# Performance work log

Hardware: AMD Instinct MI355X
Metric: run time of the kernel (lower is better)

Reference implementation:

```python
import jax, jax.numpy as jnp
import numpy as np

OMEGA = 32  # recall threshold from init_kwargs


def setup_inputs() -> dict:
    key = jax.random.key(0)
    B, T, F, H = 32, 1024, 256, 256
    stdv = 1.0 / np.sqrt(H).astype(np.float32)
    ks = jax.random.split(key, 10)
    u = lambda k, shape: jax.random.uniform(k, shape, jnp.float32, -stdv, stdv)
    return {
        "x": jax.random.normal(ks[0], (B, T, F), jnp.float32),
        "W": u(ks[1], (F, 4 * H)),
        "U": u(ks[2], (H, 4 * H)),
        "P": u(ks[3], (B, 2 * B)),
        "B_bias": u(ks[4], (4 * H,)),
        "W_r": u(ks[5], (F, 1)),
        "P_r": u(ks[6], (1, B)),
        "U_r": u(ks[7], (H, 1)),
        "W_out": u(ks[8], (H, 1)),
        "b_out": u(ks[9], (1,)),
    }


def reference(x, W, U, P, B_bias, W_r, P_r, U_r, W_out, b_out):
    Bsz, T, F = x.shape
    H = U.shape[0]
    xs = jnp.swapaxes(x, 0, 1)  # [T, B, F]
    h0 = jnp.zeros((Bsz, H), x.dtype)
    c0 = jnp.zeros((Bsz, H), x.dtype)
    Xm0 = jnp.zeros((T, Bsz, F), x.dtype)  # states_array: stored x_t per step
    Hm0 = jnp.zeros((T, Bsz, H), x.dtype)  # states_array: stored h_t per step

    def step(carry, inp):
        h, c, Xm, Hm = carry
        x_t, t = inp  # x_t: [B, F], t: scalar int (== len(states_array) before append)
        # recall gate: sigmoid(P_r @ (x_t @ W_r + h @ U_r)) -> [1,1]
        gate = jax.nn.sigmoid(P_r @ (x_t @ W_r + h @ U_r))[0, 0]
        # best index = round(t * gate); clip to valid range (source would IndexError at t)
        idx = jnp.clip(jnp.round(t.astype(x.dtype) * gate).astype(jnp.int32), 0, jnp.maximum(t - 1, 0))
        use_self = t < OMEGA
        x_rec = jnp.where(use_self, x_t, Xm[idx])
        h_rec = jnp.where(use_self, h, Hm[idx])
        # append current (x_t, h_t) to the memory bank
        Xm = Xm.at[t].set(x_t)
        Hm = Hm.at[t].set(h)
        # x_t_prime = [x_t; x_rec] (2B rows); fold the vstack into a concat of the two affine maps
        a_cur = x_t @ W + h @ U      # [B, 4H]
        a_rec = x_rec @ W + h_rec @ U  # [B, 4H]
        gates = P @ jnp.concatenate([a_cur, a_rec], axis=0) + B_bias  # [B, 4H]
        i_t, f_t, g_t, _o_raw = jnp.split(gates, 4, axis=1)
        i_t = jax.nn.sigmoid(i_t)
        f_t = jax.nn.sigmoid(f_t)
        g_t = jnp.tanh(g_t)
        o_t = i_t  # faithful to source: o_t = sigmoid(i chunk), not the o chunk
        c = f_t * c + i_t * g_t
        h = o_t * jnp.tanh(c)
        return (h, c, Xm, Hm), None

    (h, c, _, _), _ = jax.lax.scan(step, (h0, c0, Xm0, Hm0), (xs, jnp.arange(T)))
    return h @ W_out + b_out  # [B, 1]
```

## Files before the change

kernel.cpp:

```cpp
#include <hip/hip_runtime.h>
#include <cstdint>
#include <cstddef>


#define T_STEPS 1024
#define BSZ 32
#define FDIM 256
#define HDIM 256
#define G3W 384
#define KWG 64
#define HS 4
#define JC 12
#define HPAD 260
#define OMEGA 32
#define HSLICE 8192

static const size_t AXC_BYTES = (size_t)KWG * T_STEPS * G3W * sizeof(float);
static const size_t HB_BYTES  = (size_t)(T_STEPS + 1) * HSLICE * sizeof(float);
static const size_t GX_BYTES  = (size_t)T_STEPS * sizeof(double);
static const size_t GP_BYTES  = (size_t)(T_STEPS + 1) * 128 * sizeof(double);

__device__ __forceinline__ uint32_t uminv(uint32_t a, uint32_t b) {
  return a < b ? a : b;
}

__global__ __launch_bounds__(256) void phaseA(const float* __restrict__ x,
                                              const float* __restrict__ W,
                                              const float* __restrict__ W_r,
                                              const float* __restrict__ P_r,
                                              float* __restrict__ AXc,
                                              double* __restrict__ gx) {
  const int t = blockIdx.x;
  const int tid = threadIdx.x;
  __shared__ __align__(16) float xs[BSZ][HPAD];
  __shared__ double sred[BSZ];

  for (int i = tid; i < BSZ * FDIM / 4; i += 256) {
    const int b = (i * 4) >> 8;
    const int k = (i * 4) & 255;
    *(float4*)&xs[b][k] = *(const float4*)&x[((size_t)b * T_STEPS + t) * FDIM + k];
  }
  __syncthreads();

  for (int pass = 0; pass < 3; ++pass) {
    const int j = pass * 256 + tid;
    float acc[BSZ];
#pragma unroll
    for (int b = 0; b < BSZ; ++b) acc[b] = 0.f;
    for (int k0 = 0; k0 < FDIM; k0 += 4) {
      const float w0 = W[(size_t)(k0 + 0) * 1024 + j];
      const float w1 = W[(size_t)(k0 + 1) * 1024 + j];
      const float w2 = W[(size_t)(k0 + 2) * 1024 + j];
      const float w3 = W[(size_t)(k0 + 3) * 1024 + j];
#pragma unroll
      for (int b = 0; b < BSZ; ++b) {
        const float4 xv = *(const float4*)&xs[b][k0];
        acc[b] = fmaf(xv.x, w0, acc[b]);
        acc[b] = fmaf(xv.y, w1, acc[b]);
        acc[b] = fmaf(xv.z, w2, acc[b]);
        acc[b] = fmaf(xv.w, w3, acc[b]);
      }
    }
    const int wgj = (j >> 2) & 63;
    const int slot = ((j >> 8) << 2) | (j & 3);
    float* dst = AXc + ((size_t)wgj * T_STEPS + t) * G3W + slot;
    for (int b = 0; b < BSZ; ++b) dst[b * 12] = acc[b];
  }

  if (tid < BSZ) {
    double s = 0.0;
    for (int k = 0; k < FDIM; k += 4) {
      const float4 xv = *(const float4*)&xs[tid][k];
      const float4 wv = *(const float4*)&W_r[k];
      s = fma((double)xv.x, (double)wv.x, s);
      s = fma((double)xv.y, (double)wv.y, s);
      s = fma((double)xv.z, (double)wv.z, s);
      s = fma((double)xv.w, (double)wv.w, s);
    }
    sred[tid] = s;
  }
  __syncthreads();
  if (tid == 0) {
    double g = 0.0;
    for (int b = 0; b < BSZ; ++b) g = fma((double)P_r[b], sred[b], g);
    gx[t] = g;
  }
}

__global__ __launch_bounds__(256) void phaseB(const float* __restrict__ U,
                                              const float* __restrict__ P,
                                              const float* __restrict__ B_bias,
                                              const float* __restrict__ P_r,
                                              const float* __restrict__ U_r,
                                              float* __restrict__ AXc,
                                              float* __restrict__ hbank,
                                              const double* __restrict__ gx,
                                              double* __restrict__ gp) {
  const int wg = blockIdx.x;
  const int tid = threadIdx.x;
  const int lane = tid & 63;

  __shared__ __align__(16) float ULt[JC][HPAD];
  __shared__ __align__(16) float hL[BSZ][HPAD];
  __shared__ __align__(16) float PL[BSZ][64];
  __shared__ __align__(16) float acs[JC][36];
  __shared__ __align__(16) float ars[JC][36];
  __shared__ __align__(16) float red1[BSZ][JC];
  __shared__ float biasL[JC];

  for (int i = tid; i < JC * HDIM; i += 256) {
    const int jc = i >> 8, k = i & 255;
    const int col = (jc >> 2) * HDIM + wg * HS + (jc & 3);
    ULt[jc][k] = U[(size_t)k * 1024 + col];
  }
  for (int i = tid; i < BSZ * 64; i += 256) PL[i >> 6][i & 63] = P[i];
  if (tid < JC) biasL[tid] = B_bias[(tid >> 2) * HDIM + wg * HS + (tid & 3)];

  double wgt = 0.0;
  if (tid < 128) {
    wgt = (double)P_r[tid >> 2] * (double)U_r[wg * HS + (tid & 3)];
  }

  const int u = (tid >= 64) ? (tid - 64) : 0;
  const int khalf = u / 96;
  const int rmap = u % 96;
  const int jcp = rmap % 6, bA = rmap / 6;
  const int jc0 = 2 * jcp, jc1 = jc0 + 1;
  const int bB = bA + 16;
  const int kb = khalf * 128;

  const int ob = tid >> 2, ohc = tid & 3;
  const int grow = tid & 31;
  const int gc0 = (tid >> 5) * 4;

  float* __restrict__ AXwg = AXc + (size_t)wg * T_STEPS * G3W;

  float creg = 0.f;
  __syncthreads();

  for (int t = 0; t < T_STEPS; ++t) {
    float2 xwA = {0.f, 0.f}, xwB = {0.f, 0.f};
    size_t aA = 0, aB = 0;
    if (tid >= 64 && tid < 160) {
      aA = (size_t)t * G3W + bA * JC + jc0;
      aB = (size_t)t * G3W + bB * JC + jc0;
      xwA = *(const float2*)&AXwg[aA];
      xwB = *(const float2*)&AXwg[aB];
    }
    double gxt = 0.0;
    if (tid == 0) gxt = gx[t];

    {
      const uint64_t base =
          (uint64_t)(hbank + (size_t)t * HSLICE) + (uint64_t)tid * 16u;
      const uint64_t a0 = base;
      const uint64_t a1 = base + 4096u;
      const uint64_t a2 = base + 8192u;
      const uint64_t a3 = base + 12288u;
      const uint64_t a4 = base + 16384u;
      const uint64_t a5 = base + 20480u;
      const uint64_t a6 = base + 24576u;
      const uint64_t a7 = base + 28672u;
      float4 r0, r1, r2, r3, r4, r5, r6, r7;
      int guard = 0;
      for (;;) {
        asm volatile(
            "global_load_dwordx4 %0, %8, off sc0 sc1\n\t"
            "global_load_dwordx4 %1, %9, off sc0 sc1\n\t"
            "global_load_dwordx4 %2, %10, off sc0 sc1\n\t"
            "global_load_dwordx4 %3, %11, off sc0 sc1\n\t"
            "global_load_dwordx4 %4, %12, off sc0 sc1\n\t"
            "global_load_dwordx4 %5, %13, off sc0 sc1\n\t"
            "global_load_dwordx4 %6, %14, off sc0 sc1\n\t"
            "global_load_dwordx4 %7, %15, off sc0 sc1\n\t"
            "s_waitcnt vmcnt(0)"
            : "=&v"(r0), "=&v"(r1), "=&v"(r2), "=&v"(r3),
              "=&v"(r4), "=&v"(r5), "=&v"(r6), "=&v"(r7)
            : "v"(a0), "v"(a1), "v"(a2), "v"(a3),
              "v"(a4), "v"(a5), "v"(a6), "v"(a7)
            : "memory");
        uint32_t m = 0xFFFFFFFFu;
#define CHK(f) m = uminv(m, ~__float_as_uint(f))
        CHK(r0.x); CHK(r0.y); CHK(r0.z); CHK(r0.w);
        CHK(r1.x); CHK(r1.y); CHK(r1.z); CHK(r1.w);
        CHK(r2.x); CHK(r2.y); CHK(r2.z); CHK(r2.w);
        CHK(r3.x); CHK(r3.y); CHK(r3.z); CHK(r3.w);
        CHK(r4.x); CHK(r4.y); CHK(r4.z); CHK(r4.w);
        CHK(r5.x); CHK(r5.y); CHK(r5.z); CHK(r5.w);
        CHK(r6.x); CHK(r6.y); CHK(r6.z); CHK(r6.w);
        CHK(r7.x); CHK(r7.y); CHK(r7.z); CHK(r7.w);
#undef CHK
        if (m != 0u) break;
        if (++guard > (1 << 16)) break;
        __builtin_amdgcn_s_sleep(1);
      }
      *(float4*)&hL[grow][gc0 + 0]   = r0;
      *(float4*)&hL[grow][gc0 + 32]  = r1;
      *(float4*)&hL[grow][gc0 + 64]  = r2;
      *(float4*)&hL[grow][gc0 + 96]  = r3;
      *(float4*)&hL[grow][gc0 + 128] = r4;
      *(float4*)&hL[grow][gc0 + 160] = r5;
      *(float4*)&hL[grow][gc0 + 192] = r6;
      *(float4*)&hL[grow][gc0 + 224] = r7;
    }
    __syncthreads();

    float s00 = 0.f, s01 = 0.f, s10 = 0.f, s11 = 0.f;
    if (tid < 64) {
      if (t >= OMEGA) {
        const uint64_t ga0 = (uint64_t)(gp + (size_t)t * 128 + lane);
        const uint64_t ga1 = ga0 + 512u;
        double d0, d1;
        int guard = 0;
        for (;;) {
          asm volatile(
              "global_load_dwordx2 %0, %2, off sc0 sc1\n\t"
              "global_load_dwordx2 %1, %3, off sc0 sc1\n\t"
              "s_waitcnt vmcnt(0)"
              : "=&v"(d0), "=&v"(d1)
              : "v"(ga0), "v"(ga1)
              : "memory");
          const int ok = (__double_as_longlong(d0) != -1ll) &&
                         (__double_as_longlong(d1) != -1ll);
          if (__all(ok)) break;
          if (++guard > (1 << 16)) break;
          __builtin_amdgcn_s_sleep(1);
        }
        double v = d0 + d1;
        v += __shfl_xor(v, 32, 64);
        v += __shfl_xor(v, 16, 64);
        v += __shfl_xor(v, 8, 64);
        v += __shfl_xor(v, 4, 64);
        v += __shfl_xor(v, 2, 64);
        v += __shfl_xor(v, 1, 64);
        int idx = 0;
        if (tid == 0) {
          const double g = gxt + v;
          const double gate = 1.0 / (1.0 + exp(-g));
          idx = (int)rint((double)t * gate);
          if (idx > t - 1) idx = t - 1;
          if (idx < 0) idx = 0;
        }
        idx = __shfl(idx, 0, 64);
        const float* __restrict__ src = AXwg + (size_t)idx * G3W;
        float av[6];
#pragma unroll
        for (int j = 0; j < 6; ++j) av[j] = src[lane + j * 64];
#pragma unroll
        for (int j = 0; j < 6; ++j) {
          const int f = lane + j * 64;
          ars[f % JC][f / JC] = av[j];
        }
      }
    } else {
      for (int k = kb; k < kb + 128; k += 4) {
        const float4 u0 = *(const float4*)&ULt[jc0][k];
        const float4 u1 = *(const float4*)&ULt[jc1][k];
        const float4 h0 = *(const float4*)&hL[bA][k];
        const float4 h1 = *(const float4*)&hL[bB][k];
        s00 = fmaf(h0.x, u0.x, s00); s00 = fmaf(h0.y, u0.y, s00);
        s00 = fmaf(h0.z, u0.z, s00); s00 = fmaf(h0.w, u0.w, s00);
        s01 = fmaf(h0.x, u1.x, s01); s01 = fmaf(h0.y, u1.y, s01);
        s01 = fmaf(h0.z, u1.z, s01); s01 = fmaf(h0.w, u1.w, s01);
        s10 = fmaf(h1.x, u0.x, s10); s10 = fmaf(h1.y, u0.y, s10);
        s10 = fmaf(h1.z, u0.z, s10); s10 = fmaf(h1.w, u0.w, s10);
        s11 = fmaf(h1.x, u1.x, s11); s11 = fmaf(h1.y, u1.y, s11);
        s11 = fmaf(h1.z, u1.z, s11); s11 = fmaf(h1.w, u1.w, s11);
      }
      if (khalf == 1) {
        *(float2*)&red1[bA][jc0] = make_float2(s00, s01);
        *(float2*)&red1[bB][jc0] = make_float2(s10, s11);
      }
    }
    __syncthreads();

    if (tid >= 64 && tid < 160) {
      const float2 rA = *(const float2*)&red1[bA][jc0];
      const float2 rB = *(const float2*)&red1[bB][jc0];
      const float v00 = s00 + rA.x + xwA.x;
      const float v01 = s01 + rA.y + xwA.y;
      const float v10 = s10 + rB.x + xwB.x;
      const float v11 = s11 + rB.y + xwB.y;
      *(float2*)&AXwg[aA] = make_float2(v00, v01);
      *(float2*)&AXwg[aB] = make_float2(v10, v11);
      acs[jc0][bA] = v00;  acs[jc1][bA] = v01;
      acs[jc0][bB] = v10;  acs[jc1][bB] = v11;
      if (t < OMEGA) {
        ars[jc0][bA] = v00;  ars[jc1][bA] = v01;
        ars[jc0][bB] = v10;  ars[jc1][bB] = v11;
      }
    }
    __syncthreads();

    if (tid < BSZ * HS) {
      float gi = biasL[ohc];
      float gf = biasL[4 + ohc];
      float gg = biasL[8 + ohc];
#pragma unroll
      for (int b4 = 0; b4 < BSZ; b4 += 4) {
        const float4 pv = *(const float4*)&PL[ob][b4];
        const float4 ai = *(const float4*)&acs[ohc][b4];
        const float4 af = *(const float4*)&acs[4 + ohc][b4];
        const float4 ag = *(const float4*)&acs[8 + ohc][b4];
        gi = fmaf(pv.x, ai.x, gi); gi = fmaf(pv.y, ai.y, gi);
        gi = fmaf(pv.z, ai.z, gi); gi = fmaf(pv.w, ai.w, gi);
        gf = fmaf(pv.x, af.x, gf); gf = fmaf(pv.y, af.y, gf);
        gf = fmaf(pv.z, af.z, gf); gf = fmaf(pv.w, af.w, gf);
        gg = fmaf(pv.x, ag.x, gg); gg = fmaf(pv.y, ag.y, gg);
        gg = fmaf(pv.z, ag.z, gg); gg = fmaf(pv.w, ag.w, gg);
      }
#pragma unroll
      for (int b4 = 0; b4 < BSZ; b4 += 4) {
        const float4 pv = *(const float4*)&PL[ob][BSZ + b4];
        const float4 ai = *(const float4*)&ars[ohc][b4];
        const float4 af = *(const float4*)&ars[4 + ohc][b4];
        const float4 ag = *(const float4*)&ars[8 + ohc][b4];
        gi = fmaf(pv.x, ai.x, gi); gi = fmaf(pv.y, ai.y, gi);
        gi = fmaf(pv.z, ai.z, gi); gi = fmaf(pv.w, ai.w, gi);
        gf = fmaf(pv.x, af.x, gf); gf = fmaf(pv.y, af.y, gf);
        gf = fmaf(pv.z, af.z, gf); gf = fmaf(pv.w, af.w, gf);
        gg = fmaf(pv.x, ag.x, gg); gg = fmaf(pv.y, ag.y, gg);
        gg = fmaf(pv.z, ag.z, gg); gg = fmaf(pv.w, ag.w, gg);
      }
      const float iv = 1.f / (1.f + expf(-gi));
      const float fv = 1.f / (1.f + expf(-gf));
      const float gv = tanhf(gg);
      creg = fmaf(fv, creg, iv * gv);
      const float hv = iv * tanhf(creg);
      const uint64_t daddr =
          (uint64_t)(hbank + (size_t)(t + 1) * HSLICE + (size_t)wg * (BSZ * HS)) +
          (uint64_t)tid * 4u;
      asm volatile("global_store_dword %0, %1, off sc0 sc1"
                   :: "v"(daddr), "v"(hv)
                   : "memory");
      double p = wgt * (double)hv;
      p += __shfl_xor(p, 32, 64);
      p += __shfl_xor(p, 16, 64);
      p += __shfl_xor(p, 8, 64);
      p += __shfl_xor(p, 4, 64);
      p += __shfl_xor(p, 2, 64);
      p += __shfl_xor(p, 1, 64);
      if (lane == 0) {
        const uint64_t pa =
            (uint64_t)(gp + (size_t)(t + 1) * 128 + (size_t)((tid >> 6) * 64 + wg));
        asm volatile("global_store_dwordx2 %0, %1, off sc0 sc1"
                     :: "v"(pa), "v"(p)
                     : "memory");
      }
    }
  }
}

__global__ void outK(const float* __restrict__ hbank, const float* __restrict__ W_out,
                     const float* __restrict__ b_out, float* __restrict__ out) {
  const int b = threadIdx.x;
  if (b < BSZ) {
    const float* h = hbank + (size_t)T_STEPS * HSLICE;
    float s = 0.f;
    for (int wg = 0; wg < KWG; ++wg) {
      const float4 hv = *(const float4*)&h[wg * (BSZ * HS) + b * HS];
      const float4 wv = *(const float4*)&W_out[wg * HS];
      s = fmaf(hv.x, wv.x, s); s = fmaf(hv.y, wv.y, s);
      s = fmaf(hv.z, wv.z, s); s = fmaf(hv.w, wv.w, s);
    }
    out[b] = s + b_out[0];
  }
}

extern "C" void kernel_launch(void* const* d_in, const int* in_sizes, int n_in,
                              void* d_out, int out_size, void* d_ws, size_t ws_size,
                              hipStream_t stream) {
  const float* x      = (const float*)d_in[0];
  const float* W      = (const float*)d_in[1];
  const float* U      = (const float*)d_in[2];
  const float* P      = (const float*)d_in[3];
  const float* B_bias = (const float*)d_in[4];
  const float* W_r    = (const float*)d_in[5];
  const float* P_r    = (const float*)d_in[6];
  const float* U_r    = (const float*)d_in[7];
  const float* W_out  = (const float*)d_in[8];
  const float* b_out  = (const float*)d_in[9];

  char* ws = (char*)d_ws;
  float*    AXc   = (float*)ws;
  float*    hbank = (float*)(ws + AXC_BYTES);
  double*   gx    = (double*)(ws + AXC_BYTES + HB_BYTES);
  double*   gp    = (double*)(ws + AXC_BYTES + HB_BYTES + GX_BYTES);

  hipMemsetAsync(hbank, 0xFF, HB_BYTES, stream);
  hipMemsetAsync(gp, 0xFF, GP_BYTES, stream);
  hipMemsetAsync(hbank, 0, (size_t)HSLICE * sizeof(float), stream);

  phaseA<<<T_STEPS, 256, 0, stream>>>(x, W, W_r, P_r, AXc, gx);
  phaseB<<<KWG, 256, 0, stream>>>(U, P, B_bias, P_r, U_r, AXc, hbank, gx, gp);
  outK<<<1, 64, 0, stream>>>(hbank, W_out, b_out, (float*)d_out);
}
```

Before: 5.008 ms.

## Split recurrent step across 128 workgroups with two hidden columns each

Doubles the number of persistent workgroups in the recurrent phase from 64 to 128, halving each workgroup's slice of hidden units (and gate columns) per step. The hidden-state bank is also reorganized to a natural [batch][hidden] layout so each workgroup writes strided single columns and readers load contiguous rows. This aims to cut per-step compute latency on the serial critical path by spreading work across more CUs. The cost is more cross-workgroup polling traffic and synchronization participants, plus many idle threads within each workgroup.

```diff
diff --git a/kernel.cpp b/kernel.cpp
--- a/kernel.cpp
+++ b/kernel.cpp
@@ -7,10 +7,10 @@
 #define BSZ 32
 #define FDIM 256
 #define HDIM 256
-#define G3W 384
-#define KWG 64
-#define HS 4
-#define JC 12
+#define KWG 128
+#define HS 2
+#define JC 6
+#define G3W 192
 #define HPAD 260
 #define OMEGA 32
 #define HSLICE 8192
@@ -18,7 +18,7 @@
 static const size_t AXC_BYTES = (size_t)KWG * T_STEPS * G3W * sizeof(float);
 static const size_t HB_BYTES  = (size_t)(T_STEPS + 1) * HSLICE * sizeof(float);
 static const size_t GX_BYTES  = (size_t)T_STEPS * sizeof(double);
-static const size_t GP_BYTES  = (size_t)(T_STEPS + 1) * 128 * sizeof(double);
+static const size_t GP_BYTES  = (size_t)(T_STEPS + 1) * KWG * sizeof(double);
 
 __device__ __forceinline__ uint32_t uminv(uint32_t a, uint32_t b) {
   return a < b ? a : b;
@@ -61,10 +61,10 @@
         acc[b] = fmaf(xv.w, w3, acc[b]);
       }
     }
-    const int wgj = (j >> 2) & 63;
-    const int slot = ((j >> 8) << 2) | (j & 3);
+    const int wgj = (j >> 1) & 127;
+    const int slot = ((j >> 8) << 1) | (j & 1);
     float* dst = AXc + ((size_t)wgj * T_STEPS + t) * G3W + slot;
-    for (int b = 0; b < BSZ; ++b) dst[b * 12] = acc[b];
+    for (int b = 0; b < BSZ; ++b) dst[b * JC] = acc[b];
   }
 
   if (tid < BSZ) {
@@ -102,36 +102,38 @@
 
   __shared__ __align__(16) float ULt[JC][HPAD];
   __shared__ __align__(16) float hL[BSZ][HPAD];
-  __shared__ __align__(16) float PL[BSZ][64];
+  __shared__ __align__(16) float PL[BSZ][68];
   __shared__ __align__(16) float acs[JC][36];
   __shared__ __align__(16) float ars[JC][36];
-  __shared__ __align__(16) float red1[BSZ][JC];
+  __shared__ __align__(16) float red1[BSZ][8];
   __shared__ float biasL[JC];
 
   for (int i = tid; i < JC * HDIM; i += 256) {
     const int jc = i >> 8, k = i & 255;
-    const int col = (jc >> 2) * HDIM + wg * HS + (jc & 3);
+    const int col = (jc >> 1) * HDIM + wg * HS + (jc & 1);
     ULt[jc][k] = U[(size_t)k * 1024 + col];
   }
   for (int i = tid; i < BSZ * 64; i += 256) PL[i >> 6][i & 63] = P[i];
-  if (tid < JC) biasL[tid] = B_bias[(tid >> 2) * HDIM + wg * HS + (tid & 3)];
-
-  double wgt = 0.0;
-  if (tid < 128) {
-    wgt = (double)P_r[tid >> 2] * (double)U_r[wg * HS + (tid & 3)];
-  }
-
-  const int u = (tid >= 64) ? (tid - 64) : 0;
-  const int khalf = u / 96;
-  const int rmap = u % 96;
-  const int jcp = rmap % 6, bA = rmap / 6;
+  if (tid < JC) biasL[tid] = B_bias[(tid >> 1) * HDIM + wg * HS + (tid & 1)];
+
+  const bool hu_act = (tid >= 64 && tid < 160);
+  const int u = hu_act ? (tid - 64) : 0;
+  const int khalf = u / 48;
+  const int rmap = u % 48;
+  const int jcp = rmap % 3, bA = rmap / 3;
   const int jc0 = 2 * jcp, jc1 = jc0 + 1;
   const int bB = bA + 16;
   const int kb = khalf * 128;
 
-  const int ob = tid >> 2, ohc = tid & 3;
-  const int grow = tid & 31;
-  const int gc0 = (tid >> 5) * 4;
+  const int o = (tid >= 192) ? (tid - 192) : 0;
+  const int ob = o >> 1, ohc = o & 1;
+  double wgt = 0.0;
+  if (tid >= 192) {
+    wgt = (double)P_r[ob] * (double)U_r[wg * HS + ohc];
+  }
+
+  const int gw4 = tid >> 6;
+  const int gcol = (tid & 63) * 4;
 
   float* __restrict__ AXwg = AXc + (size_t)wg * T_STEPS * G3W;
 
@@ -141,7 +143,7 @@
   for (int t = 0; t < T_STEPS; ++t) {
     float2 xwA = {0.f, 0.f}, xwB = {0.f, 0.f};
     size_t aA = 0, aB = 0;
-    if (tid >= 64 && tid < 160) {
+    if (tid >= 64 && tid < 112) {
       aA = (size_t)t * G3W + bA * JC + jc0;
       aB = (size_t)t * G3W + bB * JC + jc0;
       xwA = *(const float2*)&AXwg[aA];
@@ -194,21 +196,21 @@
         if (++guard > (1 << 16)) break;
         __builtin_amdgcn_s_sleep(1);
       }
-      *(float4*)&hL[grow][gc0 + 0]   = r0;
-      *(float4*)&hL[grow][gc0 + 32]  = r1;
-      *(float4*)&hL[grow][gc0 + 64]  = r2;
-      *(float4*)&hL[grow][gc0 + 96]  = r3;
-      *(float4*)&hL[grow][gc0 + 128] = r4;
-      *(float4*)&hL[grow][gc0 + 160] = r5;
-      *(float4*)&hL[grow][gc0 + 192] = r6;
-      *(float4*)&hL[grow][gc0 + 224] = r7;
+      *(float4*)&hL[0 * 4 + gw4][gcol] = r0;
+      *(float4*)&hL[1 * 4 + gw4][gcol] = r1;
+      *(float4*)&hL[2 * 4 + gw4][gcol] = r2;
+      *(float4*)&hL[3 * 4 + gw4][gcol] = r3;
+      *(float4*)&hL[4 * 4 + gw4][gcol] = r4;
+      *(float4*)&hL[5 * 4 + gw4][gcol] = r5;
+      *(float4*)&hL[6 * 4 + gw4][gcol] = r6;
+      *(float4*)&hL[7 * 4 + gw4][gcol] = r7;
     }
     __syncthreads();
 
     float s00 = 0.f, s01 = 0.f, s10 = 0.f, s11 = 0.f;
     if (tid < 64) {
       if (t >= OMEGA) {
-        const uint64_t ga0 = (uint64_t)(gp + (size_t)t * 128 + lane);
+        const uint64_t ga0 = (uint64_t)(gp + (size_t)t * KWG + lane);
         const uint64_t ga1 = ga0 + 512u;
         double d0, d1;
         int guard = 0;
@@ -243,16 +245,16 @@
         }
         idx = __shfl(idx, 0, 64);
         const float* __restrict__ src = AXwg + (size_t)idx * G3W;
-        float av[6];
-#pragma unroll
-        for (int j = 0; j < 6; ++j) av[j] = src[lane + j * 64];
-#pragma unroll
-        for (int j = 0; j < 6; ++j) {
+        float av[3];
+#pragma unroll
+        for (int j = 0; j < 3; ++j) av[j] = src[lane + j * 64];
+#pragma unroll
+        for (int j = 0; j < 3; ++j) {
           const int f = lane + j * 64;
           ars[f % JC][f / JC] = av[j];
         }
       }
-    } else {
+    } else if (hu_act) {
       for (int k = kb; k < kb + 128; k += 4) {
         const float4 u0 = *(const float4*)&ULt[jc0][k];
         const float4 u1 = *(const float4*)&ULt[jc1][k];
@@ -274,7 +276,7 @@
     }
     __syncthreads();
 
-    if (tid >= 64 && tid < 160) {
+    if (tid >= 64 && tid < 112) {
       const float2 rA = *(const float2*)&red1[bA][jc0];
       const float2 rB = *(const float2*)&red1[bB][jc0];
       const float v00 = s00 + rA.x + xwA.x;
@@ -292,16 +294,16 @@
     }
     __syncthreads();
 
-    if (tid < BSZ * HS) {
+    if (tid >= 192) {
       float gi = biasL[ohc];
-      float gf = biasL[4 + ohc];
-      float gg = biasL[8 + ohc];
+      float gf = biasL[2 + ohc];
+      float gg = biasL[4 + ohc];
 #pragma unroll
       for (int b4 = 0; b4 < BSZ; b4 += 4) {
         const float4 pv = *(const float4*)&PL[ob][b4];
         const float4 ai = *(const float4*)&acs[ohc][b4];
-        const float4 af = *(const float4*)&acs[4 + ohc][b4];
-        const float4 ag = *(const float4*)&acs[8 + ohc][b4];
+        const float4 af = *(const float4*)&acs[2 + ohc][b4];
+        const float4 ag = *(const float4*)&acs[4 + ohc][b4];
         gi = fmaf(pv.x, ai.x, gi); gi = fmaf(pv.y, ai.y, gi);
         gi = fmaf(pv.z, ai.z, gi); gi = fmaf(pv.w, ai.w, gi);
         gf = fmaf(pv.x, af.x, gf); gf = fmaf(pv.y, af.y, gf);
@@ -313,8 +315,8 @@
       for (int b4 = 0; b4 < BSZ; b4 += 4) {
         const float4 pv = *(const float4*)&PL[ob][BSZ + b4];
         const float4 ai = *(const float4*)&ars[ohc][b4];
-        const float4 af = *(const float4*)&ars[4 + ohc][b4];
-        const float4 ag = *(const float4*)&ars[8 + ohc][b4];
+        const float4 af = *(const float4*)&ars[2 + ohc][b4];
+        const float4 ag = *(const float4*)&ars[4 + ohc][b4];
         gi = fmaf(pv.x, ai.x, gi); gi = fmaf(pv.y, ai.y, gi);
         gi = fmaf(pv.z, ai.z, gi); gi = fmaf(pv.w, ai.w, gi);
         gf = fmaf(pv.x, af.x, gf); gf = fmaf(pv.y, af.y, gf);
@@ -328,8 +330,8 @@
       creg = fmaf(fv, creg, iv * gv);
       const float hv = iv * tanhf(creg);
       const uint64_t daddr =
-          (uint64_t)(hbank + (size_t)(t + 1) * HSLICE + (size_t)wg * (BSZ * HS)) +
-          (uint64_t)tid * 4u;
+          (uint64_t)(hbank + (size_t)(t + 1) * HSLICE +
+                     (size_t)ob * HDIM + (size_t)wg * HS + ohc) ;
       asm volatile("global_store_dword %0, %1, off sc0 sc1"
                    :: "v"(daddr), "v"(hv)
                    : "memory");
@@ -341,8 +343,7 @@
       p += __shfl_xor(p, 2, 64);
       p += __shfl_xor(p, 1, 64);
       if (lane == 0) {
-        const uint64_t pa =
-            (uint64_t)(gp + (size_t)(t + 1) * 128 + (size_t)((tid >> 6) * 64 + wg));
+        const uint64_t pa = (uint64_t)(gp + (size_t)(t + 1) * KWG + wg);
         asm volatile("global_store_dwordx2 %0, %1, off sc0 sc1"
                      :: "v"(pa), "v"(p)
                      : "memory");
@@ -355,11 +356,11 @@
                      const float* __restrict__ b_out, float* __restrict__ out) {
   const int b = threadIdx.x;
   if (b < BSZ) {
-    const float* h = hbank + (size_t)T_STEPS * HSLICE;
+    const float* h = hbank + (size_t)T_STEPS * HSLICE + (size_t)b * HDIM;
     float s = 0.f;
-    for (int wg = 0; wg < KWG; ++wg) {
-      const float4 hv = *(const float4*)&h[wg * (BSZ * HS) + b * HS];
-      const float4 wv = *(const float4*)&W_out[wg * HS];
+    for (int c = 0; c < HDIM; c += 4) {
+      const float4 hv = *(const float4*)&h[c];
+      const float4 wv = *(const float4*)&W_out[c];
       s = fmaf(hv.x, wv.x, s); s = fmaf(hv.y, wv.y, s);
       s = fmaf(hv.z, wv.z, s); s = fmaf(hv.w, wv.w, s);
     }
```

After: 8.445 ms. +68.6%, slower.

## Prefetch next step's hidden-state slice on idle threads and pad LDS rows

Applied to the files above, without the earlier changes.

The spin-wait gather of the full h slice from the global bank moves off the start of every step. Threads 128-255, which take no part in publishing h, now run it at the end of the previous step. Each of these threads issues twice as many 16-byte acquire loads, covering the work the full block did before. The shared arrays hL and PL get wider row padding, presumably to cut LDS bank conflicts. This aims to shorten the serial critical path of each recurrent step, but it depends on hL no longer being read by other threads when the early gather overwrites it.

```diff
diff --git a/kernel.cpp b/kernel.cpp
--- a/kernel.cpp
+++ b/kernel.cpp
@@ -12,6 +12,7 @@
 #define HS 4
 #define JC 12
 #define HPAD 260
+#define HPADH 276
 #define OMEGA 32
 #define HSLICE 8192
 
@@ -101,8 +102,8 @@
   const int lane = tid & 63;
 
   __shared__ __align__(16) float ULt[JC][HPAD];
-  __shared__ __align__(16) float hL[BSZ][HPAD];
-  __shared__ __align__(16) float PL[BSZ][64];
+  __shared__ __align__(16) float hL[BSZ][HPADH];
+  __shared__ __align__(16) float PL[BSZ][68];
   __shared__ __align__(16) float acs[JC][36];
   __shared__ __align__(16) float ars[JC][36];
   __shared__ __align__(16) float red1[BSZ][JC];
@@ -130,13 +131,89 @@
   const int kb = khalf * 128;
 
   const int ob = tid >> 2, ohc = tid & 3;
-  const int grow = tid & 31;
-  const int gc0 = (tid >> 5) * 4;
+  const int tp = (tid >= 128) ? (tid - 128) : 0;
+  const int grow = tp & 31;
+  const int gc0 = (tp >> 5) * 4;
 
   float* __restrict__ AXwg = AXc + (size_t)wg * T_STEPS * G3W;
 
   float creg = 0.f;
   __syncthreads();
+
+#define GATHER_SLICE(TS)                                                       \
+  {                                                                            \
+    const uint64_t base =                                                      \
+        (uint64_t)(hbank + (size_t)(TS)*HSLICE) + (uint64_t)tp * 16u;          \
+    const uint64_t a0 = base;                                                  \
+    const uint64_t a1 = base + 4096u;                                          \
+    const uint64_t a2 = base + 8192u;                                          \
+    const uint64_t a3 = base + 12288u;                                         \
+    const uint64_t a4 = base + 16384u;                                         \
+    const uint64_t a5 = base + 20480u;                                         \
+    const uint64_t a6 = base + 24576u;                                         \
+    const uint64_t a7 = base + 28672u;                                         \
+    float4 r0, r1, r2, r3, r4, r5, r6, r7;                                     \
+    float4 s0, s1, s2, s3, s4, s5, s6, s7;                                     \
+    int guard = 0;                                                             \
+    for (;;) {                                                                 \
+      asm volatile(                                                            \
+          "global_load_dwordx4 %0, %16, off sc0 sc1\n\t"                       \
+          "global_load_dwordx4 %1, %16, off offset:2048 sc0 sc1\n\t"           \
+          "global_load_dwordx4 %2, %17, off sc0 sc1\n\t"                       \
+          "global_load_dwordx4 %3, %17, off offset:2048 sc0 sc1\n\t"           \
+          "global_load_dwordx4 %4, %18, off sc0 sc1\n\t"                       \
+          "global_load_dwordx4 %5, %18, off offset:2048 sc0 sc1\n\t"           \
+          "global_load_dwordx4 %6, %19, off sc0 sc1\n\t"                       \
+          "global_load_dwordx4 %7, %19, off offset:2048 sc0 sc1\n\t"           \
+          "global_load_dwordx4 %8, %20, off sc0 sc1\n\t"                       \
+          "global_load_dwordx4 %9, %20, off offset:2048 sc0 sc1\n\t"           \
+          "global_load_dwordx4 %10, %21, off sc0 sc1\n\t"                      \
+          "global_load_dwordx4 %11, %21, off offset:2048 sc0 sc1\n\t"          \
+          "global_load_dwordx4 %12, %22, off sc0 sc1\n\t"                      \
+          "global_load_dwordx4 %13, %22, off offset:2048 sc0 sc1\n\t"          \
+          "global_load_dwordx4 %14, %23, off sc0 sc1\n\t"                      \
+          "global_load_dwordx4 %15, %23, off offset:2048 sc0 sc1\n\t"          \
+          "s_waitcnt vmcnt(0)"                                                 \
+          : "=&v"(r0), "=&v"(s0), "=&v"(r1), "=&v"(s1),                        \
+            "=&v"(r2), "=&v"(s2), "=&v"(r3), "=&v"(s3),                        \
+            "=&v"(r4), "=&v"(s4), "=&v"(r5), "=&v"(s5),                        \
+            "=&v"(r6), "=&v"(s6), "=&v"(r7), "=&v"(s7)                         \
+          : "v"(a0), "v"(a1), "v"(a2), "v"(a3),                                \
+            "v"(a4), "v"(a5), "v"(a6), "v"(a7)                                 \
+          : "memory");                                                         \
+      uint32_t m = 0xFFFFFFFFu;                                                \
+      { const float4* rr[16] = {&r0,&s0,&r1,&s1,&r2,&s2,&r3,&s3,               \
+                                &r4,&s4,&r5,&s5,&r6,&s6,&r7,&s7};              \
+        _Pragma("unroll")                                                      \
+        for (int q = 0; q < 16; ++q) {                                         \
+          m = uminv(m, ~__float_as_uint(rr[q]->x));                            \
+          m = uminv(m, ~__float_as_uint(rr[q]->y));                            \
+          m = uminv(m, ~__float_as_uint(rr[q]->z));                            \
+          m = uminv(m, ~__float_as_uint(rr[q]->w));                            \
+        } }                                                                    \
+      if (m != 0u) break;                                                      \
+      if (++guard > (1 << 16)) break;         \
+      __builtin_amdgcn_s_sleep(1);                                             \
+    }                                                                          \
+    *(float4*)&hL[grow][gc0 + 0]   = r0;                                       \
+    *(float4*)&hL[grow][gc0 + 16]  = s0;                                       \
+    *(float4*)&hL[grow][gc0 + 32]  = r1;                                       \
+    *(float4*)&hL[grow][gc0 + 48]  = s1;                                       \
+    *(float4*)&hL[grow][gc0 + 64]  = r2;                                       \
+    *(float4*)&hL[grow][gc0 + 80]  = s2;                                       \
+    *(float4*)&hL[grow][gc0 + 96]  = r3;                                       \
+    *(float4*)&hL[grow][gc0 + 112] = s3;                                       \
+    *(float4*)&hL[grow][gc0 + 128] = r4;                                       \
+    *(float4*)&hL[grow][gc0 + 144] = s4;                                       \
+    *(float4*)&hL[grow][gc0 + 160] = r5;                                       \
+    *(float4*)&hL[grow][gc0 + 176] = s5;                                       \
+    *(float4*)&hL[grow][gc0 + 192] = r6;                                       \
+    *(float4*)&hL[grow][gc0 + 208] = s6;                                       \
+    *(float4*)&hL[grow][gc0 + 224] = r7;                                       \
+    *(float4*)&hL[grow][gc0 + 240] = s7;                                       \
+  }
+
+  if (tid >= 128) { GATHER_SLICE(0) }
 
   for (int t = 0; t < T_STEPS; ++t) {
     float2 xwA = {0.f, 0.f}, xwB = {0.f, 0.f};
@@ -150,59 +227,6 @@
     double gxt = 0.0;
     if (tid == 0) gxt = gx[t];
 
-    {
-      const uint64_t base =
-          (uint64_t)(hbank + (size_t)t * HSLICE) + (uint64_t)tid * 16u;
-      const uint64_t a0 = base;
-      const uint64_t a1 = base + 4096u;
-      const uint64_t a2 = base + 8192u;
-      const uint64_t a3 = base + 12288u;
-      const uint64_t a4 = base + 16384u;
-      const uint64_t a5 = base + 20480u;
-      const uint64_t a6 = base + 24576u;
-      const uint64_t a7 = base + 28672u;
-      float4 r0, r1, r2, r3, r4, r5, r6, r7;
-      int guard = 0;
-      for (;;) {
-        asm volatile(
-            "global_load_dwordx4 %0, %8, off sc0 sc1\n\t"
-            "global_load_dwordx4 %1, %9, off sc0 sc1\n\t"
-            "global_load_dwordx4 %2, %10, off sc0 sc1\n\t"
-            "global_load_dwordx4 %3, %11, off sc0 sc1\n\t"
-            "global_load_dwordx4 %4, %12, off sc0 sc1\n\t"
-            "global_load_dwordx4 %5, %13, off sc0 sc1\n\t"
-            "global_load_dwordx4 %6, %14, off sc0 sc1\n\t"
-            "global_load_dwordx4 %7, %15, off sc0 sc1\n\t"
-            "s_waitcnt vmcnt(0)"
-            : "=&v"(r0), "=&v"(r1), "=&v"(r2), "=&v"(r3),
-              "=&v"(r4), "=&v"(r5), "=&v"(r6), "=&v"(r7)
-            : "v"(a0), "v"(a1), "v"(a2), "v"(a3),
-              "v"(a4), "v"(a5), "v"(a6), "v"(a7)
-            : "memory");
-        uint32_t m = 0xFFFFFFFFu;
-#define CHK(f) m = uminv(m, ~__float_as_uint(f))
-        CHK(r0.x); CHK(r0.y); CHK(r0.z); CHK(r0.w);
-        CHK(r1.x); CHK(r1.y); CHK(r1.z); CHK(r1.w);
-        CHK(r2.x); CHK(r2.y); CHK(r2.z); CHK(r2.w);
-        CHK(r3.x); CHK(r3.y); CHK(r3.z); CHK(r3.w);
-        CHK(r4.x); CHK(r4.y); CHK(r4.z); CHK(r4.w);
-        CHK(r5.x); CHK(r5.y); CHK(r5.z); CHK(r5.w);
-        CHK(r6.x); CHK(r6.y); CHK(r6.z); CHK(r6.w);
-        CHK(r7.x); CHK(r7.y); CHK(r7.z); CHK(r7.w);
-#undef CHK
-        if (m != 0u) break;
-        if (++guard > (1 << 16)) break;
-        __builtin_amdgcn_s_sleep(1);
-      }
-      *(float4*)&hL[grow][gc0 + 0]   = r0;
-      *(float4*)&hL[grow][gc0 + 32]  = r1;
-      *(float4*)&hL[grow][gc0 + 64]  = r2;
-      *(float4*)&hL[grow][gc0 + 96]  = r3;
-      *(float4*)&hL[grow][gc0 + 128] = r4;
-      *(float4*)&hL[grow][gc0 + 160] = r5;
-      *(float4*)&hL[grow][gc0 + 192] = r6;
-      *(float4*)&hL[grow][gc0 + 224] = r7;
-    }
     __syncthreads();
 
     float s00 = 0.f, s01 = 0.f, s10 = 0.f, s11 = 0.f;
@@ -347,8 +371,11 @@
                      :: "v"(pa), "v"(p)
                      : "memory");
       }
-    }
-  }
+    } else if (tid >= 128 && t + 1 < T_STEPS) {
+      GATHER_SLICE(t + 1)
+    }
+  }
+#undef GATHER_SLICE
 }
 
 __global__ void outK(const float* __restrict__ hbank, const float* __restrict__ W_out,
```

New measurement: 5.224 ms. 1.04x slower.

## Fuse input projection into recurrent kernel with producer blocks and flag polling

Applied to the files above, without the earlier changes.

Merges the per-timestep input projection kernel into the recurrent kernel: 64 blocks run the recurrence while 192 extra worker blocks compute x@W and the recall-gate input term per timestep, publishing them with cache-bypassing stores. The recurrent blocks poll the AXc and gx buffers (pre-filled with 0xFF sentinels) so the sequential recurrence can start before all projections finish, overlapping the two phases. This adds a large memset of AXc each call and spin-wait polling, and relies on the worker blocks being co-resident with the recurrent blocks to avoid deadlock.

```diff
diff --git a/kernel.cpp b/kernel.cpp
--- a/kernel.cpp
+++ b/kernel.cpp
@@ -9,6 +9,7 @@
 #define HDIM 256
 #define G3W 384
 #define KWG 64
+#define NWRK 192
 #define HS 4
 #define JC 12
 #define HPAD 260
@@ -24,82 +25,23 @@
   return a < b ? a : b;
 }
 
-__global__ __launch_bounds__(256) void phaseA(const float* __restrict__ x,
+__global__ __launch_bounds__(256) void fusedK(const float* __restrict__ x,
                                               const float* __restrict__ W,
                                               const float* __restrict__ W_r,
-                                              const float* __restrict__ P_r,
-                                              float* __restrict__ AXc,
-                                              double* __restrict__ gx) {
-  const int t = blockIdx.x;
-  const int tid = threadIdx.x;
-  __shared__ __align__(16) float xs[BSZ][HPAD];
-  __shared__ double sred[BSZ];
-
-  for (int i = tid; i < BSZ * FDIM / 4; i += 256) {
-    const int b = (i * 4) >> 8;
-    const int k = (i * 4) & 255;
-    *(float4*)&xs[b][k] = *(const float4*)&x[((size_t)b * T_STEPS + t) * FDIM + k];
-  }
-  __syncthreads();
-
-  for (int pass = 0; pass < 3; ++pass) {
-    const int j = pass * 256 + tid;
-    float acc[BSZ];
-#pragma unroll
-    for (int b = 0; b < BSZ; ++b) acc[b] = 0.f;
-    for (int k0 = 0; k0 < FDIM; k0 += 4) {
-      const float w0 = W[(size_t)(k0 + 0) * 1024 + j];
-      const float w1 = W[(size_t)(k0 + 1) * 1024 + j];
-      const float w2 = W[(size_t)(k0 + 2) * 1024 + j];
-      const float w3 = W[(size_t)(k0 + 3) * 1024 + j];
-#pragma unroll
-      for (int b = 0; b < BSZ; ++b) {
-        const float4 xv = *(const float4*)&xs[b][k0];
-        acc[b] = fmaf(xv.x, w0, acc[b]);
-        acc[b] = fmaf(xv.y, w1, acc[b]);
-        acc[b] = fmaf(xv.z, w2, acc[b]);
-        acc[b] = fmaf(xv.w, w3, acc[b]);
-      }
-    }
-    const int wgj = (j >> 2) & 63;
-    const int slot = ((j >> 8) << 2) | (j & 3);
-    float* dst = AXc + ((size_t)wgj * T_STEPS + t) * G3W + slot;
-    for (int b = 0; b < BSZ; ++b) dst[b * 12] = acc[b];
-  }
-
-  if (tid < BSZ) {
-    double s = 0.0;
-    for (int k = 0; k < FDIM; k += 4) {
-      const float4 xv = *(const float4*)&xs[tid][k];
-      const float4 wv = *(const float4*)&W_r[k];
-      s = fma((double)xv.x, (double)wv.x, s);
-      s = fma((double)xv.y, (double)wv.y, s);
-      s = fma((double)xv.z, (double)wv.z, s);
-      s = fma((double)xv.w, (double)wv.w, s);
-    }
-    sred[tid] = s;
-  }
-  __syncthreads();
-  if (tid == 0) {
-    double g = 0.0;
-    for (int b = 0; b < BSZ; ++b) g = fma((double)P_r[b], sred[b], g);
-    gx[t] = g;
-  }
-}
-
-__global__ __launch_bounds__(256) void phaseB(const float* __restrict__ U,
+                                              const float* __restrict__ U,
                                               const float* __restrict__ P,
                                               const float* __restrict__ B_bias,
                                               const float* __restrict__ P_r,
                                               const float* __restrict__ U_r,
                                               float* __restrict__ AXc,
                                               float* __restrict__ hbank,
-                                              const double* __restrict__ gx,
+                                              double* __restrict__ gx,
                                               double* __restrict__ gp) {
-  const int wg = blockIdx.x;
   const int tid = threadIdx.x;
   const int lane = tid & 63;
 
+  __shared__ __align__(16) float xs[BSZ][HPAD];
+  __shared__ double sred[BSZ];
   __shared__ __align__(16) float ULt[JC][HPAD];
   __shared__ __align__(16) float hL[BSZ][HPAD];
   __shared__ __align__(16) float PL[BSZ][64];
@@ -108,6 +50,74 @@
   __shared__ __align__(16) float red1[BSZ][JC];
   __shared__ float biasL[JC];
 
+  if (blockIdx.x >= KWG) {
+    const int wk = blockIdx.x - KWG;
+    for (int t = wk; t < T_STEPS; t += NWRK) {
+      for (int i = tid; i < BSZ * FDIM / 4; i += 256) {
+        const int b = (i * 4) >> 8;
+        const int k = (i * 4) & 255;
+        *(float4*)&xs[b][k] =
+            *(const float4*)&x[((size_t)b * T_STEPS + t) * FDIM + k];
+      }
+      __syncthreads();
+
+      for (int pass = 0; pass < 3; ++pass) {
+        const int j = pass * 256 + tid;
+        float acc[BSZ];
+#pragma unroll
+        for (int b = 0; b < BSZ; ++b) acc[b] = 0.f;
+        for (int k0 = 0; k0 < FDIM; k0 += 4) {
+          const float w0 = W[(size_t)(k0 + 0) * 1024 + j];
+          const float w1 = W[(size_t)(k0 + 1) * 1024 + j];
+          const float w2 = W[(size_t)(k0 + 2) * 1024 + j];
+          const float w3 = W[(size_t)(k0 + 3) * 1024 + j];
+#pragma unroll
+          for (int b = 0; b < BSZ; ++b) {
+            const float4 xv = *(const float4*)&xs[b][k0];
+            acc[b] = fmaf(xv.x, w0, acc[b]);
+            acc[b] = fmaf(xv.y, w1, acc[b]);
+            acc[b] = fmaf(xv.z, w2, acc[b]);
+            acc[b] = fmaf(xv.w, w3, acc[b]);
+          }
+        }
+        const int wgj = (j >> 2) & 63;
+        const int slot = ((j >> 8) << 2) | (j & 3);
+        float* dst = AXc + ((size_t)wgj * T_STEPS + t) * G3W + slot;
+#pragma unroll
+        for (int b = 0; b < BSZ; ++b) {
+          asm volatile("global_store_dword %0, %1, off sc0 sc1"
+                       :: "v"((uint64_t)(dst + b * 12)), "v"(acc[b])
+                       : "memory");
+        }
+      }
+
+      if (tid < BSZ) {
+        double s = 0.0;
+        for (int k = 0; k < FDIM; k += 4) {
+          const float4 xv = *(const float4*)&xs[tid][k];
+          const float4 wv = *(const float4*)&W_r[k];
+          s = fma((double)xv.x, (double)wv.x, s);
+          s = fma((double)xv.y, (double)wv.y, s);
+          s = fma((double)xv.z, (double)wv.z, s);
+          s = fma((double)xv.w, (double)wv.w, s);
+        }
+        sred[tid] = s;
+      }
+      __syncthreads();
+      if (tid == 0) {
+        double g = 0.0;
+        for (int b = 0; b < BSZ; ++b) g = fma((double)P_r[b], sred[b], g);
+        asm volatile("global_store_dwordx2 %0, %1, off sc0 sc1"
+                     :: "v"((uint64_t)(gx + t)), "v"(g)
+                     : "memory");
+      }
+      __syncthreads();
+    }
+    return;
+  }
+
+  const int wg = blockIdx.x;
+
   for (int i = tid; i < JC * HDIM; i += 256) {
     const int jc = i >> 8, k = i & 255;
     const int col = (jc >> 2) * HDIM + wg * HS + (jc & 3);
@@ -138,18 +148,32 @@
   float creg = 0.f;
   __syncthreads();
 
+  float2 xwA = {0.f, 0.f}, xwB = {0.f, 0.f};
+#define XW_POLL(TT)                                                            \
+  if (tid >= 64 && tid < 160) {                                                \
+    const uint64_t xa = (uint64_t)(AXwg + (size_t)(TT)*G3W + bA * JC + jc0);   \
+    const uint64_t xb = (uint64_t)(AXwg + (size_t)(TT)*G3W + bB * JC + jc0);   \
+    int guard = 0;                                                             \
+    for (;;) {                                                                 \
+      asm volatile("global_load_dwordx2 %0, %2, off sc0 sc1\n\t"               \
+                   "global_load_dwordx2 %1, %3, off sc0 sc1\n\t"               \
+                   "s_waitcnt vmcnt(0)"                                        \
+                   : "=&v"(xwA), "=&v"(xwB)                                    \
+                   : "v"(xa), "v"(xb)                                          \
+                   : "memory");                                                \
+      const int ok = (__float_as_uint(xwA.x) != 0xFFFFFFFFu) &&                \
+                     (__float_as_uint(xwA.y) != 0xFFFFFFFFu) &&                \
+                     (__float_as_uint(xwB.x) != 0xFFFFFFFFu) &&                \
+                     (__float_as_uint(xwB.y) != 0xFFFFFFFFu);                  \
+      if (__all(ok)) break;                                                    \
+      if (++guard > (1 << 18)) break;         \
+      __builtin_amdgcn_s_sleep(2);                                             \
+    }                                                                          \
+  }
+
+  XW_POLL(0)
+
   for (int t = 0; t < T_STEPS; ++t) {
-    float2 xwA = {0.f, 0.f}, xwB = {0.f, 0.f};
-    size_t aA = 0, aB = 0;
-    if (tid >= 64 && tid < 160) {
-      aA = (size_t)t * G3W + bA * JC + jc0;
-      aB = (size_t)t * G3W + bB * JC + jc0;
-      xwA = *(const float2*)&AXwg[aA];
-      xwB = *(const float2*)&AXwg[aB];
-    }
-    double gxt = 0.0;
-    if (tid == 0) gxt = gx[t];
-
     {
       const uint64_t base =
           (uint64_t)(hbank + (size_t)t * HSLICE) + (uint64_t)tid * 16u;
@@ -210,18 +234,21 @@
       if (t >= OMEGA) {
         const uint64_t ga0 = (uint64_t)(gp + (size_t)t * 128 + lane);
         const uint64_t ga1 = ga0 + 512u;
-        double d0, d1;
+        const uint64_t gxa = (uint64_t)(gx + t);
+        double d0, d1, gxv;
         int guard = 0;
         for (;;) {
           asm volatile(
-              "global_load_dwordx2 %0, %2, off sc0 sc1\n\t"
-              "global_load_dwordx2 %1, %3, off sc0 sc1\n\t"
+              "global_load_dwordx2 %0, %3, off sc0 sc1\n\t"
+              "global_load_dwordx2 %1, %4, off sc0 sc1\n\t"
+              "global_load_dwordx2 %2, %5, off sc0 sc1\n\t"
               "s_waitcnt vmcnt(0)"
-              : "=&v"(d0), "=&v"(d1)
-              : "v"(ga0), "v"(ga1)
+              : "=&v"(d0), "=&v"(d1), "=&v"(gxv)
+              : "v"(ga0), "v"(ga1), "v"(gxa)
               : "memory");
           const int ok = (__double_as_longlong(d0) != -1ll) &&
-                         (__double_as_longlong(d1) != -1ll);
+                         (__double_as_longlong(d1) != -1ll) &&
+                         (__double_as_longlong(gxv) != -1ll);
           if (__all(ok)) break;
           if (++guard > (1 << 16)) break;
           __builtin_amdgcn_s_sleep(1);
@@ -235,7 +262,7 @@
         v += __shfl_xor(v, 1, 64);
         int idx = 0;
         if (tid == 0) {
-          const double g = gxt + v;
+          const double g = gxv + v;
           const double gate = 1.0 / (1.0 + exp(-g));
           idx = (int)rint((double)t * gate);
           if (idx > t - 1) idx = t - 1;
@@ -275,6 +302,8 @@
     __syncthreads();
 
     if (tid >= 64 && tid < 160) {
+      const size_t aA = (size_t)t * G3W + bA * JC + jc0;
+      const size_t aB = (size_t)t * G3W + bB * JC + jc0;
       const float2 rA = *(const float2*)&red1[bA][jc0];
       const float2 rB = *(const float2*)&red1[bB][jc0];
       const float v00 = s00 + rA.x + xwA.x;
@@ -348,7 +377,9 @@
                      : "memory");
       }
     }
-  }
+    if (t + 1 < T_STEPS) { XW_POLL(t + 1) }
+  }
+#undef XW_POLL
 }
 
 __global__ void outK(const float* __restrict__ hbank, const float* __restrict__ W_out,
@@ -387,11 +418,13 @@
   double*   gx    = (double*)(ws + AXC_BYTES + HB_BYTES);
   double*   gp    = (double*)(ws + AXC_BYTES + HB_BYTES + GX_BYTES);
 
+  hipMemsetAsync(AXc, 0xFF, AXC_BYTES, stream);
   hipMemsetAsync(hbank, 0xFF, HB_BYTES, stream);
+  hipMemsetAsync(gx, 0xFF, GX_BYTES, stream);
   hipMemsetAsync(gp, 0xFF, GP_BYTES, stream);
   hipMemsetAsync(hbank, 0, (size_t)HSLICE * sizeof(float), stream);
 
-  phaseA<<<T_STEPS, 256, 0, stream>>>(x, W, W_r, P_r, AXc, gx);
-  phaseB<<<KWG, 256, 0, stream>>>(U, P, B_bias, P_r, U_r, AXc, hbank, gx, gp);
+  fusedK<<<KWG + NWRK, 256, 0, stream>>>(x, W, W_r, U, P, B_bias, P_r, U_r,
+                                         AXc, hbank, gx, gp);
   outK<<<1, 64, 0, stream>>>(hbank, W_out, b_out, (float*)d_out);
 }
```

New measurement: 4.876 ms. 1.03x faster.
